# Performance work log

Hardware: AMD Instinct MI355X
Metric: run time of the kernel (lower is better)

Reference implementation:

```python
import jax, jax.numpy as jnp
import numpy as np

LN_EPS = 1e-6

def layernorm(x, w, b):
    m = jnp.mean(x, axis=-1, keepdims=True)
    v = jnp.mean((x - m) ** 2, axis=-1, keepdims=True)
    return (x - m) * jax.lax.rsqrt(v + LN_EPS) * w + b

def rotate_half(x):
    x1, x2 = jnp.split(x, 2, axis=-1)
    return jnp.concatenate([-x2, x1], axis=-1)

def headwise_lowrank(x, U, V, b):
    # x: [B,S,D], U: [H,D,r], V: [H,r,hd] -> [B,S,H*hd]
    xu = jnp.einsum('bsd,hdr->bshr', x, U)
    y = jnp.einsum('bshr,hre->bshe', xu, V)
    B, S, H, E = y.shape
    return y.reshape(B, S, H * E) + b

def setup_inputs() -> dict:
    key = jax.random.key(0)
    B, S, D, H, HD = 4, 2048, 768, 12, 64
    RA, RF, DFF = 32, 512, 3072
    ks = jax.random.split(key, 20)
    s = 0.02
    inp = {
        'x': jax.random.normal(ks[0], (B, S, D), jnp.float32),
        'attn_norm_w': jnp.ones((D,), jnp.float32),
        'attn_norm_b': jnp.zeros((D,), jnp.float32),
        'Uq': jax.random.normal(ks[1], (H, D, RA), jnp.float32) * s,
        'Vq': jax.random.normal(ks[2], (H, RA, HD), jnp.float32),
        'bq': jax.random.normal(ks[3], (D,), jnp.float32) * s,
        'Uk': jax.random.normal(ks[4], (H, D, RA), jnp.float32) * s,
        'Vk': jax.random.normal(ks[5], (H, RA, HD), jnp.float32),
        'bk': jax.random.normal(ks[6], (D,), jnp.float32) * s,
        'Uv': jax.random.normal(ks[7], (H, D, RA), jnp.float32) * s,
        'Vv': jax.random.normal(ks[8], (H, RA, HD), jnp.float32),
        'bv': jax.random.normal(ks[9], (D,), jnp.float32) * s,
        'Wo_w': jax.random.normal(ks[10], (D, D), jnp.float32) * s,
        'Wo_b': jax.random.normal(ks[11], (D,), jnp.float32) * s,
        'mlp_norm_w': jnp.ones((D,), jnp.float32),
        'mlp_norm_b': jnp.zeros((D,), jnp.float32),
        'Ui': jax.random.normal(ks[12], (D, RF), jnp.float32) * s,
        'Vi': jax.random.normal(ks[13], (RF, 2 * DFF), jnp.float32),
        'bi': jax.random.normal(ks[14], (2 * DFF,), jnp.float32) * s,
        'Uo': jax.random.normal(ks[15], (DFF, RF), jnp.float32) * s,
        'Vo': jax.random.normal(ks[16], (RF, D), jnp.float32),
        'bo': jax.random.normal(ks[17], (D,), jnp.float32) * s,
    }
    # real RoPE tables [S, HD]
    inv_freq = 1.0 / (10000.0 ** (np.arange(0, HD, 2, dtype=np.float32) / HD))
    t = np.arange(S, dtype=np.float32)
    freqs = np.outer(t, inv_freq)  # [S, HD/2]
    emb = np.concatenate([freqs, freqs], axis=-1)
    inp['cos'] = jnp.asarray(np.cos(emb))
    inp['sin'] = jnp.asarray(np.sin(emb))
    return inp

def reference(x, attn_norm_w, attn_norm_b, Uq, Vq, bq, Uk, Vk, bk, Uv, Vv, bv,
              cos, sin, Wo_w, Wo_b, mlp_norm_w, mlp_norm_b, Ui, Vi, bi, Uo, Vo, bo):
    B, S, D = x.shape
    H, HD = Vq.shape[0], Vq.shape[2]
    # --- attention sub-block (pre-norm) ---
    h = layernorm(x, attn_norm_w, attn_norm_b)
    q = headwise_lowrank(h, Uq, Vq, bq).reshape(B, S, H, HD).transpose(0, 2, 1, 3)
    k = headwise_lowrank(h, Uk, Vk, bk).reshape(B, S, H, HD).transpose(0, 2, 1, 3)
    v = headwise_lowrank(h, Uv, Vv, bv).reshape(B, S, H, HD).transpose(0, 2, 1, 3)
    c = cos[None, None]  # [1,1,S,HD]
    s_ = sin[None, None]
    q = q * c + rotate_half(q) * s_
    k = k * c + rotate_half(k) * s_
    scale = 1.0 / jnp.sqrt(jnp.asarray(HD, q.dtype))
    scores = jnp.einsum('bhqd,bhkd->bhqk', q, k) * scale
    attn = jax.nn.softmax(scores, axis=-1)
    o = jnp.einsum('bhqk,bhkd->bhqd', attn, v)
    o = o.transpose(0, 2, 1, 3).reshape(B, S, D)
    x1 = x + o @ Wo_w.T + Wo_b
    # --- FFN sub-block (pre-norm, low-rank GEGLU) ---
    h2 = layernorm(x1, mlp_norm_w, mlp_norm_b)
    u = (h2 @ Ui) @ Vi + bi  # [B,S,2*dff]
    g1, g2 = jnp.split(u, 2, axis=-1)
    g = jax.nn.gelu(g1, approximate=True) * g2
    y = (g @ Uo) @ Vo + bo
    return x1 + y
```

## Files before the change

kernel.cpp:

```cpp
#include <hip/hip_runtime.h>
#include <hip/hip_bf16.h>
#include <math.h>

#define NTOK 8192
#define SEQ  2048
#define DM   768
#define NH   12
#define HD2  64
#define RA   32
#define NG   3072

typedef __attribute__((ext_vector_type(8))) short bf16x8;
typedef __attribute__((ext_vector_type(4))) float f32x4;

__device__ __forceinline__ float b2f(unsigned short u) {
    union { unsigned int i; float f; } v; v.i = ((unsigned int)u) << 16; return v.f;
}
__device__ __forceinline__ unsigned short f2b_rne(float f) {
    union { float f; unsigned int i; } v; v.f = f;
    unsigned int b = v.i + 0x7FFFu + ((v.i >> 16) & 1u);
    return (unsigned short)(b >> 16);
}
__device__ __forceinline__ float wval(const void* p, size_t i, int bf) {
    return bf ? b2f(((const unsigned short*)p)[i]) : ((const float*)p)[i];
}
__device__ __forceinline__ unsigned int cvt_pk_bf16(float a, float b) {
    unsigned int r;
    asm("v_cvt_pk_bf16_f32 %0, %1, %2" : "=v"(r) : "v"(a), "v"(b));
    return r;
}

__global__ void detect_kernel(const unsigned int* __restrict__ w1, int* __restrict__ flag) {
    *flag = (w1[0] == 0x3F800000u) ? 0 : 1;
}

__global__ __launch_bounds__(256) void conv_f32_kernel(const void* __restrict__ src,
        float* __restrict__ dst, int n, const int* __restrict__ flag) {
    int i = blockIdx.x * 256 + threadIdx.x;
    if (i < n)
        dst[i] = (*flag) ? b2f(((const unsigned short*)src)[i]) : ((const float*)src)[i];
}

__global__ __launch_bounds__(256) void conv_b16_kernel(const void* __restrict__ src,
        unsigned short* __restrict__ dst, int n, const int* __restrict__ flag) {
    int i = blockIdx.x * 256 + threadIdx.x;
    if (i < n)
        dst[i] = (*flag) ? ((const unsigned short*)src)[i] : f2b_rne(((const float*)src)[i]);
}

__global__ __launch_bounds__(256) void conv_split_kernel(const void* __restrict__ src,
        unsigned short* __restrict__ hi, unsigned short* __restrict__ lo,
        int n, const int* __restrict__ flag) {
    int i = blockIdx.x * 256 + threadIdx.x;
    if (i < n) {
        float v = (*flag) ? b2f(((const unsigned short*)src)[i]) : ((const float*)src)[i];
        unsigned short h = f2b_rne(v);
        hi[i] = h;
        lo[i] = f2b_rne(v - b2f(h));
    }
}

__global__ __launch_bounds__(256) void ln_kernel(const float* __restrict__ x,
        const void* __restrict__ w, const void* __restrict__ b,
        void* __restrict__ out, void* __restrict__ out2,
        const int* __restrict__ flag, int mode) {
    int bf = *flag;
    int row = blockIdx.x, tid = threadIdx.x;
    const float* xr = x + (size_t)row * DM;
    float v0 = xr[tid];
    float v1 = xr[tid + 256];
    float v2 = xr[tid + 512];
    float s = v0 + v1 + v2;
    float ss = v0 * v0 + v1 * v1 + v2 * v2;
    #pragma unroll
    for (int off = 32; off >= 1; off >>= 1) {
        s  += __shfl_xor(s, off);
        ss += __shfl_xor(ss, off);
    }
    __shared__ float rs[4], rq[4];
    int wid = tid >> 6;
    if ((tid & 63) == 0) { rs[wid] = s; rq[wid] = ss; }
    __syncthreads();
    s  = rs[0] + rs[1] + rs[2] + rs[3];
    ss = rq[0] + rq[1] + rq[2] + rq[3];
    float mean = s * (1.0f / DM);
    float var  = ss * (1.0f / DM) - mean * mean;
    float inv  = rsqrtf(var + 1e-6f);
    float o0 = (v0 - mean) * inv * wval(w, tid, bf)       + wval(b, tid, bf);
    float o1 = (v1 - mean) * inv * wval(w, tid + 256, bf) + wval(b, tid + 256, bf);
    float o2 = (v2 - mean) * inv * wval(w, tid + 512, bf) + wval(b, tid + 512, bf);
    if (mode == 2) {
        unsigned short* oh = (unsigned short*)out  + (size_t)row * DM;
        unsigned short* ol = (unsigned short*)out2 + (size_t)row * DM;
        unsigned short h0 = f2b_rne(o0), h1 = f2b_rne(o1), h2 = f2b_rne(o2);
        oh[tid] = h0; oh[tid + 256] = h1; oh[tid + 512] = h2;
        ol[tid]       = f2b_rne(o0 - b2f(h0));
        ol[tid + 256] = f2b_rne(o1 - b2f(h1));
        ol[tid + 512] = f2b_rne(o2 - b2f(h2));
    } else if (mode == 1) {
        unsigned short* orow = (unsigned short*)out + (size_t)row * DM;
        orow[tid] = f2b_rne(o0); orow[tid + 256] = f2b_rne(o1); orow[tid + 512] = f2b_rne(o2);
    } else {
        float* orow = (float*)out + (size_t)row * DM;
        orow[tid] = o0; orow[tid + 256] = o1; orow[tid + 512] = o2;
    }
}

__global__ __launch_bounds__(256) void xu_mfma(
        const unsigned short* __restrict__ Ah, const unsigned short* __restrict__ Al,
        const unsigned short* __restrict__ Uh0, const unsigned short* __restrict__ Ul0,
        const unsigned short* __restrict__ Uh1, const unsigned short* __restrict__ Ul1,
        const unsigned short* __restrict__ Uh2, const unsigned short* __restrict__ Ul2,
        float* __restrict__ XU) {
    __shared__ unsigned short Ash[128][40], Asl[128][40];
    __shared__ unsigned short Bsh[128][40], Bsl[128][40];
    int tid = threadIdx.x;
    int w = tid >> 6, lane = tid & 63;
    int n16 = lane & 15, quad = lane >> 4;
    int m0 = blockIdx.x * 128, n0 = blockIdx.y * 128;
    int which = n0 / 384;
    const unsigned short* Uh = (which == 0) ? Uh0 : (which == 1) ? Uh1 : Uh2;
    const unsigned short* Ul = (which == 0) ? Ul0 : (which == 1) ? Ul1 : Ul2;
    int nh0 = n0 - which * 384;
    int mh = (w & 1) * 64, nh = (w >> 1) * 64;
    f32x4 acc[4][4] = {};

    int am = tid >> 1, akb = (tid & 1) * 16;
    const unsigned short* ahp = Ah + (size_t)(m0 + am) * DM + akb;
    const unsigned short* alp = Al + (size_t)(m0 + am) * DM + akb;
    int kp = (tid & 15) * 2, nb = (tid >> 4) * 8;
    int hc = nh0 + nb;
    int head = hc >> 5, rr = hc & 31;
    size_t bbase = (size_t)head * (DM * RA) + (size_t)kp * RA + rr;

    uint4 rah0 = *(const uint4*)ahp,       rah1 = *(const uint4*)(ahp + 8);
    uint4 ral0 = *(const uint4*)alp,       ral1 = *(const uint4*)(alp + 8);
    uint4 rbh0 = *(const uint4*)(Uh + bbase);
    uint4 rbh1 = *(const uint4*)(Uh + bbase + RA);
    uint4 rbl0 = *(const uint4*)(Ul + bbase);
    uint4 rbl1 = *(const uint4*)(Ul + bbase + RA);

    for (int k0 = 0; k0 < DM; k0 += 32) {
        __builtin_amdgcn_s_barrier();
        *(uint4*)&Ash[am][akb]     = rah0;
        *(uint4*)&Ash[am][akb + 8] = rah1;
        *(uint4*)&Asl[am][akb]     = ral0;
        *(uint4*)&Asl[am][akb + 8] = ral1;
        {
            const unsigned int* a = (const unsigned int*)&rbh0;
            const unsigned int* b = (const unsigned int*)&rbh1;
            #pragma unroll
            for (int d = 0; d < 4; d++) {
                *(unsigned int*)&Bsh[nb + 2 * d][kp]     = (a[d] & 0xFFFFu) | (b[d] << 16);
                *(unsigned int*)&Bsh[nb + 2 * d + 1][kp] = (a[d] >> 16) | (b[d] & 0xFFFF0000u);
            }
            const unsigned int* c = (const unsigned int*)&rbl0;
            const unsigned int* e = (const unsigned int*)&rbl1;
            #pragma unroll
            for (int d = 0; d < 4; d++) {
                *(unsigned int*)&Bsl[nb + 2 * d][kp]     = (c[d] & 0xFFFFu) | (e[d] << 16);
                *(unsigned int*)&Bsl[nb + 2 * d + 1][kp] = (c[d] >> 16) | (e[d] & 0xFFFF0000u);
            }
        }
        if (k0 + 32 < DM) {
            rah0 = *(const uint4*)(ahp + k0 + 32); rah1 = *(const uint4*)(ahp + k0 + 40);
            ral0 = *(const uint4*)(alp + k0 + 32); ral1 = *(const uint4*)(alp + k0 + 40);
            size_t nbb = bbase + (size_t)(k0 + 32) * RA;
            rbh0 = *(const uint4*)(Uh + nbb); rbh1 = *(const uint4*)(Uh + nbb + RA);
            rbl0 = *(const uint4*)(Ul + nbb); rbl1 = *(const uint4*)(Ul + nbb + RA);
        }
        asm volatile("s_waitcnt lgkmcnt(0)" ::: "memory");
        __builtin_amdgcn_s_barrier();
        bf16x8 ah[4], al[4], bh[4], bl[4];
        #pragma unroll
        for (int i = 0; i < 4; i++) {
            ah[i] = *(const bf16x8*)&Ash[mh + i * 16 + n16][quad * 8];
            al[i] = *(const bf16x8*)&Asl[mh + i * 16 + n16][quad * 8];
            bh[i] = *(const bf16x8*)&Bsh[nh + i * 16 + n16][quad * 8];
            bl[i] = *(const bf16x8*)&Bsl[nh + i * 16 + n16][quad * 8];
        }
        #pragma unroll
        for (int mi = 0; mi < 4; mi++)
            #pragma unroll
            for (int ni = 0; ni < 4; ni++) {
                acc[mi][ni] = __builtin_amdgcn_mfma_f32_16x16x32_bf16(ah[mi], bh[ni], acc[mi][ni], 0, 0, 0);
                acc[mi][ni] = __builtin_amdgcn_mfma_f32_16x16x32_bf16(ah[mi], bl[ni], acc[mi][ni], 0, 0, 0);
                acc[mi][ni] = __builtin_amdgcn_mfma_f32_16x16x32_bf16(al[mi], bh[ni], acc[mi][ni], 0, 0, 0);
            }
    }
    #pragma unroll
    for (int mi = 0; mi < 4; mi++)
        #pragma unroll
        for (int ni = 0; ni < 4; ni++) {
            int col = n0 + nh + ni * 16 + n16;
            #pragma unroll
            for (int r = 0; r < 4; r++) {
                int row = m0 + mh + mi * 16 + quad * 4 + r;
                XU[(size_t)row * 1152 + col] = acc[mi][ni][r];
            }
        }
}

__global__ __launch_bounds__(256) void qkv2_kernel(
        const float* __restrict__ XU,
        const void* __restrict__ Vq, const void* __restrict__ bq,
        const void* __restrict__ Vk, const void* __restrict__ bk,
        const void* __restrict__ Vv, const void* __restrict__ bv,
        const void* __restrict__ cosT, const void* __restrict__ sinT,
        unsigned short* __restrict__ qhg, unsigned short* __restrict__ qlg,
        unsigned short* __restrict__ khg, unsigned short* __restrict__ klg,
        unsigned short* __restrict__ vtg, const int* __restrict__ flag) {
    int bf = *flag;
    int tok0 = blockIdx.x * 64;
    int head = blockIdx.y;
    int tid = threadIdx.x;
    int row = tid >> 2;
    int e0  = (tid & 3) * 16;
    int tok = tok0 + row;
    int bb = tok >> 11, ssp = tok & (SEQ - 1);
    int ssp0 = tok0 & (SEQ - 1);
    int bh = bb * NH + head;
    __shared__ float XUs[64][33];
    __shared__ float Vws[32][65];
    __shared__ float obs[64][65];
    const void* Vp[3] = {Vq, Vk, Vv};
    const void* bp[3] = {bq, bk, bv};
    for (int which = 0; which < 3; which++) {
        __syncthreads();
        for (int i = tid; i < 2048; i += 256) {
            int rr = i >> 5, r = i & 31;
            XUs[rr][r] = XU[(size_t)(tok0 + rr) * 1152 + which * 384 + head * 32 + r];
        }
        for (int i = tid; i < 2048; i += 256) {
            int r = i >> 6, e = i & 63;
            Vws[r][e] = wval(Vp[which], (size_t)head * RA * HD2 + (size_t)r * 64 + e, bf);
        }
        __syncthreads();
        float acc[16];
        #pragma unroll
        for (int j = 0; j < 16; j++) acc[j] = wval(bp[which], head * 64 + e0 + j, bf);
        #pragma unroll 8
        for (int r = 0; r < 32; r++) {
            float xv = XUs[row][r];
            #pragma unroll
            for (int j = 0; j < 16; j++) acc[j] += xv * Vws[r][e0 + j];
        }
        #pragma unroll
        for (int j = 0; j < 16; j++) obs[row][e0 + j] = acc[j];
        __syncthreads();
        if (which == 2) {
            int e = tid >> 2, seg = (tid & 3) * 16;
            unsigned short buf[16];
            #pragma unroll
            for (int i = 0; i < 16; i++) buf[i] = f2b_rne(obs[seg + i][e]);
            unsigned short* dp = vtg + ((size_t)bh * 64 + e) * SEQ + ssp0 + seg;
            *(uint4*)dp = ((const uint4*)buf)[0];
            *(uint4*)(dp + 8) = ((const uint4*)buf)[1];
        } else {
            float scale = (which == 0) ? 0.18033688011112042f : 1.0f;
            unsigned short hbuf[16], lbuf[16];
            #pragma unroll
            for (int j = 0; j < 16; j++) {
                int e = e0 + j;
                float c  = wval(cosT, (size_t)ssp * 64 + e, bf);
                float sn = wval(sinT, (size_t)ssp * 64 + e, bf);
                float other = (e < 32) ? -obs[row][e + 32] : obs[row][e - 32];
                float val = (acc[j] * c + other * sn) * scale;
                unsigned short h = f2b_rne(val);
                hbuf[j] = h;
                lbuf[j] = f2b_rne(val - b2f(h));
            }
            unsigned short* hp = ((which == 0) ? qhg : khg) + ((size_t)bh * SEQ + ssp) * 64 + e0;
            unsigned short* lp = ((which == 0) ? qlg : klg) + ((size_t)bh * SEQ + ssp) * 64 + e0;
            *(uint4*)hp = ((const uint4*)hbuf)[0];
            *(uint4*)(hp + 8) = ((const uint4*)hbuf)[1];
            *(uint4*)lp = ((const uint4*)lbuf)[0];
            *(uint4*)(lp + 8) = ((const uint4*)lbuf)[1];
        }
    }
}

__global__ __launch_bounds__(256) void attn_mfma(
        const unsigned short* __restrict__ qh, const unsigned short* __restrict__ ql,
        const unsigned short* __restrict__ kh, const unsigned short* __restrict__ kl,
        const unsigned short* __restrict__ vt, unsigned short* __restrict__ og) {
    int qt = blockIdx.x, bh = blockIdx.y;
    int bb = bh / NH, hh = bh - bb * NH;
    int tid = threadIdx.x;
    int w = tid >> 6, lane = tid & 63;
    int n16 = lane & 15, quad = lane >> 4;

    __shared__ __align__(16) unsigned short Khs[64][64];
    __shared__ __align__(16) unsigned short Kls[64][64];
    __shared__ __align__(16) unsigned short VTs[64][64];
    __shared__ __align__(16) unsigned short Pbs[4][16][64];

    size_t qoff = ((size_t)bh * SEQ + qt * 64 + w * 16 + n16) * 64 + quad * 8;
    bf16x8 aqh0 = *(const bf16x8*)(qh + qoff);
    bf16x8 aqh1 = *(const bf16x8*)(qh + qoff + 32);
    bf16x8 aql0 = *(const bf16x8*)(ql + qoff);
    bf16x8 aql1 = *(const bf16x8*)(ql + qoff + 32);

    bf16x8 vones;
    #pragma unroll
    for (int i = 0; i < 8; i++) vones[i] = (short)0x3F80;

    float m[4] = {-1e30f, -1e30f, -1e30f, -1e30f};
    float l[4] = {0.f, 0.f, 0.f, 0.f};
    f32x4 O[4] = {};
    const unsigned short* kh_p = kh + (size_t)bh * SEQ * 64;
    const unsigned short* kl_p = kl + (size_t)bh * SEQ * 64;
    const unsigned short* vt_p = vt + (size_t)bh * 64 * SEQ;

    int row0 = tid >> 3, ch = tid & 7;
    int row1 = row0 + 32;
    int sw0 = (ch ^ (row0 & 7)) * 8;
    int sw1 = (ch ^ (row1 & 7)) * 8;
    size_t ko0 = (size_t)row0 * 64 + ch * 8;
    size_t ko1 = (size_t)row1 * 64 + ch * 8;
    size_t vo0 = (size_t)row0 * SEQ + ch * 8;
    size_t vo1 = (size_t)row1 * SEQ + ch * 8;

    uint4 rkh0 = *(const uint4*)(kh_p + ko0);
    uint4 rkh1 = *(const uint4*)(kh_p + ko1);
    uint4 rkl0 = *(const uint4*)(kl_p + ko0);
    uint4 rkl1 = *(const uint4*)(kl_p + ko1);
    uint4 rv0  = *(const uint4*)(vt_p + vo0);
    uint4 rv1  = *(const uint4*)(vt_p + vo1);

    int px = n16 & 7;
    int c0 = (quad ^ px) * 8;
    int c1 = ((quad + 4) ^ px) * 8;

    for (int t0 = 0; t0 < SEQ; t0 += 64) {
        __builtin_amdgcn_s_barrier();
        *(uint4*)&Khs[row0][sw0] = rkh0;
        *(uint4*)&Khs[row1][sw1] = rkh1;
        *(uint4*)&Kls[row0][sw0] = rkl0;
        *(uint4*)&Kls[row1][sw1] = rkl1;
        *(uint4*)&VTs[row0][sw0] = rv0;
        *(uint4*)&VTs[row1][sw1] = rv1;
        if (t0 + 64 < SEQ) {
            size_t kt = (size_t)(t0 + 64) * 64;
            rkh0 = *(const uint4*)(kh_p + kt + ko0);
            rkh1 = *(const uint4*)(kh_p + kt + ko1);
            rkl0 = *(const uint4*)(kl_p + kt + ko0);
            rkl1 = *(const uint4*)(kl_p + kt + ko1);
            rv0  = *(const uint4*)(vt_p + (t0 + 64) + vo0);
            rv1  = *(const uint4*)(vt_p + (t0 + 64) + vo1);
        }
        asm volatile("s_waitcnt lgkmcnt(0)" ::: "memory");
        __builtin_amdgcn_s_barrier();

        f32x4 s[4];
        #pragma unroll
        for (int t = 0; t < 4; t++) {
            int rr = 16 * t + n16;
            bf16x8 bkh0 = *(const bf16x8*)&Khs[rr][c0];
            bf16x8 bkh1 = *(const bf16x8*)&Khs[rr][c1];
            bf16x8 bkl0 = *(const bf16x8*)&Kls[rr][c0];
            bf16x8 bkl1 = *(const bf16x8*)&Kls[rr][c1];
            f32x4 a = {};
            a = __builtin_amdgcn_mfma_f32_16x16x32_bf16(aqh0, bkh0, a, 0, 0, 0);
            a = __builtin_amdgcn_mfma_f32_16x16x32_bf16(aqh1, bkh1, a, 0, 0, 0);
            a = __builtin_amdgcn_mfma_f32_16x16x32_bf16(aqh0, bkl0, a, 0, 0, 0);
            a = __builtin_amdgcn_mfma_f32_16x16x32_bf16(aqh1, bkl1, a, 0, 0, 0);
            a = __builtin_amdgcn_mfma_f32_16x16x32_bf16(aql0, bkh0, a, 0, 0, 0);
            a = __builtin_amdgcn_mfma_f32_16x16x32_bf16(aql1, bkh1, a, 0, 0, 0);
            s[t] = a;
        }
        float mt[4];
        #pragma unroll
        for (int r = 0; r < 4; r++) {
            float v = fmaxf(fmaxf(s[0][r], s[1][r]), fmaxf(s[2][r], s[3][r]));
            v = fmaxf(v, __shfl_xor(v, 1));
            v = fmaxf(v, __shfl_xor(v, 2));
            v = fmaxf(v, __shfl_xor(v, 4));
            v = fmaxf(v, __shfl_xor(v, 8));
            mt[r] = v;
        }
        float need = fmaxf(fmaxf(mt[0] - m[0], mt[1] - m[1]),
                           fmaxf(mt[2] - m[2], mt[3] - m[3]));
        if (__any(need > 8.0f)) {
            #pragma unroll
            for (int r = 0; r < 4; r++) {
                float mn = fmaxf(m[r], mt[r]);
                float al = exp2f(m[r] - mn);
                m[r] = mn;
                l[r] *= al;
                #pragma unroll
                for (int t2 = 0; t2 < 4; t2++) O[t2][r] *= al;
            }
        }
        int qr = quad * 4;
        #pragma unroll
        for (int t = 0; t < 4; t++) {
            float p0 = exp2f(s[t][0] - m[0]);
            float p1 = exp2f(s[t][1] - m[1]);
            float p2 = exp2f(s[t][2] - m[2]);
            float p3 = exp2f(s[t][3] - m[3]);
            unsigned int pk01 = cvt_pk_bf16(p0, p1);
            unsigned int pk23 = cvt_pk_bf16(p2, p3);
            int cb = 2 * t + (n16 >> 3);
            Pbs[w][qr + 0][((cb ^ ((qr + 0) & 7)) << 3) | px] = (unsigned short)pk01;
            Pbs[w][qr + 1][((cb ^ ((qr + 1) & 7)) << 3) | px] = (unsigned short)(pk01 >> 16);
            Pbs[w][qr + 2][((cb ^ ((qr + 2) & 7)) << 3) | px] = (unsigned short)pk23;
            Pbs[w][qr + 3][((cb ^ ((qr + 3) & 7)) << 3) | px] = (unsigned short)(pk23 >> 16);
        }
        bf16x8 ap0 = *(const bf16x8*)&Pbs[w][n16][c0];
        bf16x8 ap1 = *(const bf16x8*)&Pbs[w][n16][c1];
        f32x4 ls = {};
        ls = __builtin_amdgcn_mfma_f32_16x16x32_bf16(ap0, vones, ls, 0, 0, 0);
        ls = __builtin_amdgcn_mfma_f32_16x16x32_bf16(ap1, vones, ls, 0, 0, 0);
        #pragma unroll
        for (int r = 0; r < 4; r++) l[r] += ls[r];
        #pragma unroll
        for (int t2 = 0; t2 < 4; t2++) {
            bf16x8 bv0 = *(const bf16x8*)&VTs[16 * t2 + n16][c0];
            bf16x8 bv1 = *(const bf16x8*)&VTs[16 * t2 + n16][c1];
            O[t2] = __builtin_amdgcn_mfma_f32_16x16x32_bf16(ap0, bv0, O[t2], 0, 0, 0);
            O[t2] = __builtin_amdgcn_mfma_f32_16x16x32_bf16(ap1, bv1, O[t2], 0, 0, 0);
        }
    }
    int srow = qt * 64 + w * 16 + quad * 4;
    #pragma unroll
    for (int r = 0; r < 4; r++) {
        float inv = 1.0f / l[r];
        unsigned short* op = og + ((size_t)bb * SEQ + srow + r) * DM + hh * HD2 + n16;
        #pragma unroll
        for (int t2 = 0; t2 < 4; t2++)
            op[16 * t2] = f2b_rne(O[t2][r] * inv);
    }
}

template <int MODE, bool TB>
__global__ __launch_bounds__(512) void gemm_bf16(
        const unsigned short* __restrict__ A, const unsigned short* __restrict__ Bw,
        const void* __restrict__ bias, const float* __restrict__ resid,
        void* __restrict__ Cout, int Nn, int K, const int* __restrict__ flag) {
    __shared__ unsigned short As[128][40];
    __shared__ unsigned short Bs[128][40];
    int tid = threadIdx.x;
    int w = tid >> 6, lane = tid & 63;
    int n16 = lane & 15, quad = lane >> 4;
    int m0 = blockIdx.x * 128, n0 = blockIdx.y * 128;
    int mh = (w & 3) * 32, nh = (w >> 2) * 64;
    f32x4 acc[2][4] = {};

    int st = tid & 255;
    bool isA = tid < 256;
    int am = st >> 1, akb = (st & 1) * 16;
    int bkp = (st & 15) * 2, bnb = (st >> 4) * 8;
    int bn = st >> 1, bkb = (st & 1) * 16;
    const unsigned short* gp0;
    const unsigned short* gp1;
    if (isA) {
        gp0 = A + (size_t)(m0 + am) * K + akb;
        gp1 = gp0 + 8;
    } else if (!TB) {
        gp0 = Bw + (size_t)bkp * Nn + n0 + bnb;
        gp1 = gp0 + Nn;
    } else {
        gp0 = Bw + (size_t)(n0 + bn) * K + bkb;
        gp1 = gp0 + 8;
    }
    uint4 r0 = *(const uint4*)gp0;
    uint4 r1 = *(const uint4*)gp1;

    for (int k0 = 0; k0 < K; k0 += 32) {
        __builtin_amdgcn_s_barrier();
        if (isA) {
            *(uint4*)&As[am][akb]     = r0;
            *(uint4*)&As[am][akb + 8] = r1;
        } else if (!TB) {
            const unsigned int* a = (const unsigned int*)&r0;
            const unsigned int* b = (const unsigned int*)&r1;
            #pragma unroll
            for (int d = 0; d < 4; d++) {
                *(unsigned int*)&Bs[bnb + 2 * d][bkp]     = (a[d] & 0xFFFFu) | (b[d] << 16);
                *(unsigned int*)&Bs[bnb + 2 * d + 1][bkp] = (a[d] >> 16) | (b[d] & 0xFFFF0000u);
            }
        } else {
            *(uint4*)&Bs[bn][bkb]     = r0;
            *(uint4*)&Bs[bn][bkb + 8] = r1;
        }
        if (k0 + 32 < K) {
            size_t adv = (isA || TB) ? (size_t)(k0 + 32) : (size_t)(k0 + 32) * Nn;
            r0 = *(const uint4*)(gp0 + adv);
            r1 = *(const uint4*)(gp1 + adv);
        }
        asm volatile("s_waitcnt lgkmcnt(0)" ::: "memory");
        __builtin_amdgcn_s_barrier();
        bf16x8 af[2], bfr[4];
        #pragma unroll
        for (int i = 0; i < 2; i++)
            af[i] = *(const bf16x8*)&As[mh + i * 16 + n16][quad * 8];
        #pragma unroll
        for (int i = 0; i < 4; i++)
            bfr[i] = *(const bf16x8*)&Bs[nh + i * 16 + n16][quad * 8];
        #pragma unroll
        for (int mi = 0; mi < 2; mi++)
            #pragma unroll
            for (int ni = 0; ni < 4; ni++)
                acc[mi][ni] = __builtin_amdgcn_mfma_f32_16x16x32_bf16(af[mi], bfr[ni], acc[mi][ni], 0, 0, 0);
    }
    int bf = (MODE == 0) ? 0 : *flag;
    #pragma unroll
    for (int ni = 0; ni < 4; ni++) {
        int col = n0 + nh + ni * 16 + n16;
        float bv = (MODE == 0) ? 0.f : wval(bias, col, bf);
        #pragma unroll
        for (int mi = 0; mi < 2; mi++) {
            #pragma unroll
            for (int r = 0; r < 4; r++) {
                int row = m0 + mh + mi * 16 + quad * 4 + r;
                float val = acc[mi][ni][r];
                if constexpr (MODE == 0) {
                    ((unsigned short*)Cout)[(size_t)row * Nn + col] = f2b_rne(val);
                } else if constexpr (MODE == 1) {
                    ((float*)Cout)[(size_t)row * Nn + col] =
                        val + bv + resid[(size_t)row * Nn + col];
                } else {
                    float o = val + bv + resid[(size_t)row * Nn + col];
                    if (bf)
                        ((unsigned short*)Cout)[(size_t)row * Nn + col] = f2b_rne(o);
                    else
                        ((float*)Cout)[(size_t)row * Nn + col] = o;
                }
            }
        }
    }
}

__global__ __launch_bounds__(256) void geglu_bf16(
        const unsigned short* __restrict__ A, const unsigned short* __restrict__ Bw,
        const void* __restrict__ bias, unsigned short* __restrict__ G,
        const int* __restrict__ flag) {
    int bf = *flag;
    const int K = 512, Nn = 2 * NG;
    __shared__ unsigned short As[128][40];
    __shared__ unsigned short B1s[64][40];
    __shared__ unsigned short B2s[64][40];
    int tid = threadIdx.x;
    int w = tid >> 6, lane = tid & 63;
    int n16 = lane & 15, quad = lane >> 4;
    int m0 = blockIdx.x * 128, n0 = blockIdx.y * 64;
    int mh = (w & 1) * 64;
    int nq = (w >> 1) * 32;
    f32x4 acc1[4][2] = {}, acc2[4][2] = {};

    int am = tid >> 1, akb = (tid & 1) * 16;
    const unsigned short* aptr = A + (size_t)(m0 + am) * K + akb;
    uint4 ra0 = *(const uint4*)aptr;
    uint4 ra1 = *(const uint4*)(aptr + 8);
    int t_ = tid & 127, hsel = tid >> 7;
    int bkp = (t_ & 15) * 2, bnb = (t_ >> 4) * 8;
    const unsigned short* bptr = Bw + (size_t)bkp * Nn + n0 + (size_t)hsel * NG + bnb;
    uint4 rb0 = *(const uint4*)bptr;
    uint4 rb1 = *(const uint4*)(bptr + Nn);

    for (int k0 = 0; k0 < K; k0 += 32) {
        __builtin_amdgcn_s_barrier();
        *(uint4*)&As[am][akb]     = ra0;
        *(uint4*)&As[am][akb + 8] = ra1;
        {
            const unsigned int* a = (const unsigned int*)&rb0;
            const unsigned int* b = (const unsigned int*)&rb1;
            unsigned short (*Bst)[40] = hsel ? B2s : B1s;
            #pragma unroll
            for (int d = 0; d < 4; d++) {
                *(unsigned int*)&Bst[bnb + 2 * d][bkp]     = (a[d] & 0xFFFFu) | (b[d] << 16);
                *(unsigned int*)&Bst[bnb + 2 * d + 1][bkp] = (a[d] >> 16) | (b[d] & 0xFFFF0000u);
            }
        }
        if (k0 + 32 < K) {
            ra0 = *(const uint4*)(aptr + k0 + 32);
            ra1 = *(const uint4*)(aptr + k0 + 40);
            const unsigned short* nbp = bptr + (size_t)(k0 + 32) * Nn;
            rb0 = *(const uint4*)nbp;
            rb1 = *(const uint4*)(nbp + Nn);
        }
        asm volatile("s_waitcnt lgkmcnt(0)" ::: "memory");
        __builtin_amdgcn_s_barrier();
        bf16x8 af[4], b1f[2], b2f_[2];
        #pragma unroll
        for (int i = 0; i < 4; i++)
            af[i] = *(const bf16x8*)&As[mh + i * 16 + n16][quad * 8];
        #pragma unroll
        for (int i = 0; i < 2; i++) {
            b1f[i]  = *(const bf16x8*)&B1s[nq + i * 16 + n16][quad * 8];
            b2f_[i] = *(const bf16x8*)&B2s[nq + i * 16 + n16][quad * 8];
        }
        #pragma unroll
        for (int mi = 0; mi < 4; mi++)
            #pragma unroll
            for (int ni = 0; ni < 2; ni++) {
                acc1[mi][ni] = __builtin_amdgcn_mfma_f32_16x16x32_bf16(af[mi], b1f[ni], acc1[mi][ni], 0, 0, 0);
                acc2[mi][ni] = __builtin_amdgcn_mfma_f32_16x16x32_bf16(af[mi], b2f_[ni], acc2[mi][ni], 0, 0, 0);
            }
    }
    #pragma unroll
    for (int ni = 0; ni < 2; ni++) {
        int ccol = nq + ni * 16 + n16;
        float b1 = wval(bias, n0 + ccol, bf);
        float b2 = wval(bias, NG + n0 + ccol, bf);
        #pragma unroll
        for (int mi = 0; mi < 4; mi++) {
            #pragma unroll
            for (int r = 0; r < 4; r++) {
                int rrow = mh + mi * 16 + quad * 4 + r;
                float u1 = acc1[mi][ni][r] + b1;
                float u2 = acc2[mi][ni][r] + b2;
                float nz = fminf(-2.3022083f * (u1 + 0.044715f * u1 * u1 * u1), 126.f);
                float gl = u1 * __builtin_amdgcn_rcpf(1.0f + exp2f(nz));
                G[(size_t)(m0 + rrow) * NG + n0 + ccol] = f2b_rne(gl * u2);
            }
        }
    }
}

extern "C" void kernel_launch(void* const* d_in, const int* in_sizes, int n_in,
                              void* d_out, int out_size, void* d_ws, size_t ws_size,
                              hipStream_t stream) {
    (void)in_sizes; (void)n_in; (void)out_size; (void)ws_size;
    const size_t ND = (size_t)NTOK * DM;
    const int USZ = NH * DM * RA;

    float* ws = (float*)d_ws;
    int*   flag = (int*)d_ws;
    float* xf = ws + 256;
    float* P0 = xf + ND;
    float* P1 = P0 + ND;
    float* P2 = P1 + ND;
    float* P3 = P2 + ND;
    float* P4 = P3 + ND;
    float* P5 = P4 + ND;
    float* XU = P4;

    unsigned short* hH = (unsigned short*)P0;
    unsigned short* hL = hH + ND;
    unsigned short* qhb = (unsigned short*)P1;
    unsigned short* qlb = qhb + ND;
    unsigned short* khb = qhb + 2 * ND;
    unsigned short* klb = qhb + 3 * ND;
    unsigned short* vtb = qhb + 4 * ND;
    unsigned short* ob  = (unsigned short*)P0;
    unsigned short* h2b = (unsigned short*)P1;
    unsigned short* tb  = (unsigned short*)P2;
    unsigned short* gb  = (unsigned short*)P3;
    unsigned short* t2b = (unsigned short*)P0;
    unsigned short* wb  = (unsigned short*)(P5 + ND);
    unsigned short* WoB = wb;
    unsigned short* UiB = WoB + 589824;
    unsigned short* ViB = UiB + 393216;
    unsigned short* UoB = ViB + 3145728;
    unsigned short* VoB = UoB + 1572864;
    unsigned short* UqH = VoB + 393216;
    unsigned short* UqL = UqH + USZ;
    unsigned short* UkH = UqL + USZ;
    unsigned short* UkL = UkH + USZ;
    unsigned short* UvH = UkL + USZ;
    unsigned short* UvL = UvH + USZ;

    detect_kernel<<<1, 1, 0, stream>>>((const unsigned int*)d_in[1], flag);
    conv_f32_kernel<<<(int)((ND + 255) / 256), 256, 0, stream>>>(d_in[0], xf, (int)ND, flag);
    conv_b16_kernel<<<(589824 + 255) / 256, 256, 0, stream>>>(d_in[12], WoB, 589824, flag);
    conv_b16_kernel<<<(393216 + 255) / 256, 256, 0, stream>>>(d_in[16], UiB, 393216, flag);
    conv_b16_kernel<<<(3145728 + 255) / 256, 256, 0, stream>>>(d_in[17], ViB, 3145728, flag);
    conv_b16_kernel<<<(1572864 + 255) / 256, 256, 0, stream>>>(d_in[19], UoB, 1572864, flag);
    conv_b16_kernel<<<(393216 + 255) / 256, 256, 0, stream>>>(d_in[20], VoB, 393216, flag);
    conv_split_kernel<<<(USZ + 255) / 256, 256, 0, stream>>>(d_in[3], UqH, UqL, USZ, flag);
    conv_split_kernel<<<(USZ + 255) / 256, 256, 0, stream>>>(d_in[6], UkH, UkL, USZ, flag);
    conv_split_kernel<<<(USZ + 255) / 256, 256, 0, stream>>>(d_in[9], UvH, UvL, USZ, flag);

    ln_kernel<<<NTOK, 256, 0, stream>>>(xf, d_in[1], d_in[2], hH, hL, flag, 2);
    xu_mfma<<<dim3(64, 9), 256, 0, stream>>>(hH, hL, UqH, UqL, UkH, UkL, UvH, UvL, XU);
    qkv2_kernel<<<dim3(NTOK / 64, NH), 256, 0, stream>>>(XU,
                                         d_in[4], d_in[5], d_in[7], d_in[8],
                                         d_in[10], d_in[11], d_in[22], d_in[23],
                                         qhb, qlb, khb, klb, vtb, flag);
    attn_mfma<<<dim3(SEQ / 64, 4 * NH), 256, 0, stream>>>(qhb, qlb, khb, klb, vtb, ob);
    gemm_bf16<1, true><<<dim3(64, 6), 512, 0, stream>>>(ob, WoB, d_in[13], xf,
                                                        (void*)P5, DM, DM, flag);
    ln_kernel<<<NTOK, 256, 0, stream>>>(P5, d_in[14], d_in[15], (void*)h2b, nullptr, flag, 1);
    gemm_bf16<0, false><<<dim3(64, 4), 512, 0, stream>>>(h2b, UiB, nullptr, nullptr,
                                                         (void*)tb, 512, DM, flag);
    geglu_bf16<<<dim3(64, 48), 256, 0, stream>>>(tb, ViB, d_in[18], gb, flag);
    gemm_bf16<0, false><<<dim3(64, 4), 512, 0, stream>>>(gb, UoB, nullptr, nullptr,
                                                         (void*)t2b, 512, NG, flag);
    gemm_bf16<3, false><<<dim3(64, 6), 512, 0, stream>>>(t2b, VoB, d_in[21], P5,
                                                         d_out, DM, 512, flag);
}
```

Baseline: 740.2 us.

## Drop split-bf16 Q/K in attention and widen GEGLU tiles to 128x128

Q and K are now stored as a single bf16 value instead of a hi/lo bf16 pair, so the attention score loop issues 2 MFMAs per tile instead of 6, with half the K shared-memory staging and global traffic. Separately, the GEGLU GEMM uses 512-thread blocks with 128-wide N tiles and dedicated loader threads for A and B, halving the grid. The precision reduction in QK^T may raise numerical error in the attention scores against the fp32 reference.

```diff
diff --git a/kernel.cpp b/kernel.cpp
--- a/kernel.cpp
+++ b/kernel.cpp
@@ -207,8 +207,7 @@
         const void* __restrict__ Vk, const void* __restrict__ bk,
         const void* __restrict__ Vv, const void* __restrict__ bv,
         const void* __restrict__ cosT, const void* __restrict__ sinT,
-        unsigned short* __restrict__ qhg, unsigned short* __restrict__ qlg,
-        unsigned short* __restrict__ khg, unsigned short* __restrict__ klg,
+        unsigned short* __restrict__ qg, unsigned short* __restrict__ kg,
         unsigned short* __restrict__ vtg, const int* __restrict__ flag) {
     int bf = *flag;
     int tok0 = blockIdx.x * 64;
@@ -258,7 +257,7 @@
             *(uint4*)(dp + 8) = ((const uint4*)buf)[1];
         } else {
             float scale = (which == 0) ? 0.18033688011112042f : 1.0f;
-            unsigned short hbuf[16], lbuf[16];
+            unsigned short hbuf[16];
             #pragma unroll
             for (int j = 0; j < 16; j++) {
                 int e = e0 + j;
@@ -266,23 +265,17 @@
                 float sn = wval(sinT, (size_t)ssp * 64 + e, bf);
                 float other = (e < 32) ? -obs[row][e + 32] : obs[row][e - 32];
                 float val = (acc[j] * c + other * sn) * scale;
-                unsigned short h = f2b_rne(val);
-                hbuf[j] = h;
-                lbuf[j] = f2b_rne(val - b2f(h));
-            }
-            unsigned short* hp = ((which == 0) ? qhg : khg) + ((size_t)bh * SEQ + ssp) * 64 + e0;
-            unsigned short* lp = ((which == 0) ? qlg : klg) + ((size_t)bh * SEQ + ssp) * 64 + e0;
+                hbuf[j] = f2b_rne(val);
+            }
+            unsigned short* hp = ((which == 0) ? qg : kg) + ((size_t)bh * SEQ + ssp) * 64 + e0;
             *(uint4*)hp = ((const uint4*)hbuf)[0];
             *(uint4*)(hp + 8) = ((const uint4*)hbuf)[1];
-            *(uint4*)lp = ((const uint4*)lbuf)[0];
-            *(uint4*)(lp + 8) = ((const uint4*)lbuf)[1];
         }
     }
 }
 
 __global__ __launch_bounds__(256) void attn_mfma(
-        const unsigned short* __restrict__ qh, const unsigned short* __restrict__ ql,
-        const unsigned short* __restrict__ kh, const unsigned short* __restrict__ kl,
+        const unsigned short* __restrict__ qg, const unsigned short* __restrict__ kg,
         const unsigned short* __restrict__ vt, unsigned short* __restrict__ og) {
     int qt = blockIdx.x, bh = blockIdx.y;
     int bb = bh / NH, hh = bh - bb * NH;
@@ -291,15 +284,12 @@
     int n16 = lane & 15, quad = lane >> 4;
 
     __shared__ __align__(16) unsigned short Khs[64][64];
-    __shared__ __align__(16) unsigned short Kls[64][64];
     __shared__ __align__(16) unsigned short VTs[64][64];
     __shared__ __align__(16) unsigned short Pbs[4][16][64];
 
     size_t qoff = ((size_t)bh * SEQ + qt * 64 + w * 16 + n16) * 64 + quad * 8;
-    bf16x8 aqh0 = *(const bf16x8*)(qh + qoff);
-    bf16x8 aqh1 = *(const bf16x8*)(qh + qoff + 32);
-    bf16x8 aql0 = *(const bf16x8*)(ql + qoff);
-    bf16x8 aql1 = *(const bf16x8*)(ql + qoff + 32);
+    bf16x8 aq0 = *(const bf16x8*)(qg + qoff);
+    bf16x8 aq1 = *(const bf16x8*)(qg + qoff + 32);
 
     bf16x8 vones;
     #pragma unroll
@@ -308,8 +298,7 @@
     float m[4] = {-1e30f, -1e30f, -1e30f, -1e30f};
     float l[4] = {0.f, 0.f, 0.f, 0.f};
     f32x4 O[4] = {};
-    const unsigned short* kh_p = kh + (size_t)bh * SEQ * 64;
-    const unsigned short* kl_p = kl + (size_t)bh * SEQ * 64;
+    const unsigned short* k_p  = kg + (size_t)bh * SEQ * 64;
     const unsigned short* vt_p = vt + (size_t)bh * 64 * SEQ;
 
     int row0 = tid >> 3, ch = tid & 7;
@@ -321,12 +310,10 @@
     size_t vo0 = (size_t)row0 * SEQ + ch * 8;
     size_t vo1 = (size_t)row1 * SEQ + ch * 8;
 
-    uint4 rkh0 = *(const uint4*)(kh_p + ko0);
-    uint4 rkh1 = *(const uint4*)(kh_p + ko1);
-    uint4 rkl0 = *(const uint4*)(kl_p + ko0);
-    uint4 rkl1 = *(const uint4*)(kl_p + ko1);
-    uint4 rv0  = *(const uint4*)(vt_p + vo0);
-    uint4 rv1  = *(const uint4*)(vt_p + vo1);
+    uint4 rk0 = *(const uint4*)(k_p + ko0);
+    uint4 rk1 = *(const uint4*)(k_p + ko1);
+    uint4 rv0 = *(const uint4*)(vt_p + vo0);
+    uint4 rv1 = *(const uint4*)(vt_p + vo1);
 
     int px = n16 & 7;
     int c0 = (quad ^ px) * 8;
@@ -334,20 +321,16 @@
 
     for (int t0 = 0; t0 < SEQ; t0 += 64) {
         __builtin_amdgcn_s_barrier();
-        *(uint4*)&Khs[row0][sw0] = rkh0;
-        *(uint4*)&Khs[row1][sw1] = rkh1;
-        *(uint4*)&Kls[row0][sw0] = rkl0;
-        *(uint4*)&Kls[row1][sw1] = rkl1;
+        *(uint4*)&Khs[row0][sw0] = rk0;
+        *(uint4*)&Khs[row1][sw1] = rk1;
         *(uint4*)&VTs[row0][sw0] = rv0;
         *(uint4*)&VTs[row1][sw1] = rv1;
         if (t0 + 64 < SEQ) {
             size_t kt = (size_t)(t0 + 64) * 64;
-            rkh0 = *(const uint4*)(kh_p + kt + ko0);
-            rkh1 = *(const uint4*)(kh_p + kt + ko1);
-            rkl0 = *(const uint4*)(kl_p + kt + ko0);
-            rkl1 = *(const uint4*)(kl_p + kt + ko1);
-            rv0  = *(const uint4*)(vt_p + (t0 + 64) + vo0);
-            rv1  = *(const uint4*)(vt_p + (t0 + 64) + vo1);
+            rk0 = *(const uint4*)(k_p + kt + ko0);
+            rk1 = *(const uint4*)(k_p + kt + ko1);
+            rv0 = *(const uint4*)(vt_p + (t0 + 64) + vo0);
+            rv1 = *(const uint4*)(vt_p + (t0 + 64) + vo1);
         }
         asm volatile("s_waitcnt lgkmcnt(0)" ::: "memory");
         __builtin_amdgcn_s_barrier();
@@ -356,17 +339,11 @@
         #pragma unroll
         for (int t = 0; t < 4; t++) {
             int rr = 16 * t + n16;
-            bf16x8 bkh0 = *(const bf16x8*)&Khs[rr][c0];
-            bf16x8 bkh1 = *(const bf16x8*)&Khs[rr][c1];
-            bf16x8 bkl0 = *(const bf16x8*)&Kls[rr][c0];
-            bf16x8 bkl1 = *(const bf16x8*)&Kls[rr][c1];
+            bf16x8 bk0 = *(const bf16x8*)&Khs[rr][c0];
+            bf16x8 bk1 = *(const bf16x8*)&Khs[rr][c1];
             f32x4 a = {};
-            a = __builtin_amdgcn_mfma_f32_16x16x32_bf16(aqh0, bkh0, a, 0, 0, 0);
-            a = __builtin_amdgcn_mfma_f32_16x16x32_bf16(aqh1, bkh1, a, 0, 0, 0);
-            a = __builtin_amdgcn_mfma_f32_16x16x32_bf16(aqh0, bkl0, a, 0, 0, 0);
-            a = __builtin_amdgcn_mfma_f32_16x16x32_bf16(aqh1, bkl1, a, 0, 0, 0);
-            a = __builtin_amdgcn_mfma_f32_16x16x32_bf16(aql0, bkh0, a, 0, 0, 0);
-            a = __builtin_amdgcn_mfma_f32_16x16x32_bf16(aql1, bkh1, a, 0, 0, 0);
+            a = __builtin_amdgcn_mfma_f32_16x16x32_bf16(aq0, bk0, a, 0, 0, 0);
+            a = __builtin_amdgcn_mfma_f32_16x16x32_bf16(aq1, bk1, a, 0, 0, 0);
             s[t] = a;
         }
         float mt[4];
@@ -532,88 +509,110 @@
     }
 }
 
-__global__ __launch_bounds__(256) void geglu_bf16(
+__global__ __launch_bounds__(512) void geglu_bf16(
         const unsigned short* __restrict__ A, const unsigned short* __restrict__ Bw,
         const void* __restrict__ bias, unsigned short* __restrict__ G,
         const int* __restrict__ flag) {
     int bf = *flag;
     const int K = 512, Nn = 2 * NG;
     __shared__ unsigned short As[128][40];
-    __shared__ unsigned short B1s[64][40];
-    __shared__ unsigned short B2s[64][40];
+    __shared__ unsigned short B1s[128][40];
+    __shared__ unsigned short B2s[128][40];
     int tid = threadIdx.x;
     int w = tid >> 6, lane = tid & 63;
     int n16 = lane & 15, quad = lane >> 4;
-    int m0 = blockIdx.x * 128, n0 = blockIdx.y * 64;
-    int mh = (w & 1) * 64;
-    int nq = (w >> 1) * 32;
-    f32x4 acc1[4][2] = {}, acc2[4][2] = {};
-
-    int am = tid >> 1, akb = (tid & 1) * 16;
-    const unsigned short* aptr = A + (size_t)(m0 + am) * K + akb;
-    uint4 ra0 = *(const uint4*)aptr;
-    uint4 ra1 = *(const uint4*)(aptr + 8);
-    int t_ = tid & 127, hsel = tid >> 7;
+    int m0 = blockIdx.x * 128, n0 = blockIdx.y * 128;
+    int mh = (w & 3) * 32, nh = (w >> 2) * 64;
+    f32x4 acc1[2][4] = {}, acc2[2][4] = {};
+
+    bool isA = tid < 256;
+    int st = tid & 255;
+    int am = st >> 1, akb = (st & 1) * 16;
+    int t_ = tid & 127, hsel = (tid & 255) >> 7;
     int bkp = (t_ & 15) * 2, bnb = (t_ >> 4) * 8;
-    const unsigned short* bptr = Bw + (size_t)bkp * Nn + n0 + (size_t)hsel * NG + bnb;
-    uint4 rb0 = *(const uint4*)bptr;
-    uint4 rb1 = *(const uint4*)(bptr + Nn);
+    const unsigned short* gpa;
+    const unsigned short* gpb;
+    uint4 r0, r1, r2, r3;
+    if (isA) {
+        gpa = A + (size_t)(m0 + am) * K + akb;
+        r0 = *(const uint4*)gpa;
+        r1 = *(const uint4*)(gpa + 8);
+    } else {
+        gpb = Bw + (size_t)bkp * Nn + n0 + (size_t)hsel * NG + bnb;
+        r0 = *(const uint4*)gpb;
+        r1 = *(const uint4*)(gpb + Nn);
+        r2 = *(const uint4*)(gpb + 64);
+        r3 = *(const uint4*)(gpb + Nn + 64);
+    }
 
     for (int k0 = 0; k0 < K; k0 += 32) {
         __builtin_amdgcn_s_barrier();
-        *(uint4*)&As[am][akb]     = ra0;
-        *(uint4*)&As[am][akb + 8] = ra1;
-        {
-            const unsigned int* a = (const unsigned int*)&rb0;
-            const unsigned int* b = (const unsigned int*)&rb1;
+        if (isA) {
+            *(uint4*)&As[am][akb]     = r0;
+            *(uint4*)&As[am][akb + 8] = r1;
+        } else {
             unsigned short (*Bst)[40] = hsel ? B2s : B1s;
+            const unsigned int* a = (const unsigned int*)&r0;
+            const unsigned int* b = (const unsigned int*)&r1;
             #pragma unroll
             for (int d = 0; d < 4; d++) {
                 *(unsigned int*)&Bst[bnb + 2 * d][bkp]     = (a[d] & 0xFFFFu) | (b[d] << 16);
                 *(unsigned int*)&Bst[bnb + 2 * d + 1][bkp] = (a[d] >> 16) | (b[d] & 0xFFFF0000u);
             }
+            const unsigned int* c = (const unsigned int*)&r2;
+            const unsigned int* e = (const unsigned int*)&r3;
+            #pragma unroll
+            for (int d = 0; d < 4; d++) {
+                *(unsigned int*)&Bst[bnb + 64 + 2 * d][bkp]     = (c[d] & 0xFFFFu) | (e[d] << 16);
+                *(unsigned int*)&Bst[bnb + 64 + 2 * d + 1][bkp] = (c[d] >> 16) | (e[d] & 0xFFFF0000u);
+            }
         }
         if (k0 + 32 < K) {
-            ra0 = *(const uint4*)(aptr + k0 + 32);
-            ra1 = *(const uint4*)(aptr + k0 + 40);
-            const unsigned short* nbp = bptr + (size_t)(k0 + 32) * Nn;
-            rb0 = *(const uint4*)nbp;
-            rb1 = *(const uint4*)(nbp + Nn);
+            if (isA) {
+                r0 = *(const uint4*)(gpa + k0 + 32);
+                r1 = *(const uint4*)(gpa + k0 + 40);
+            } else {
+                const unsigned short* nbp = gpb + (size_t)(k0 + 32) * Nn;
+                r0 = *(const uint4*)nbp;
+                r1 = *(const uint4*)(nbp + Nn);
+                r2 = *(const uint4*)(nbp + 64);
+                r3 = *(const uint4*)(nbp + Nn + 64);
+            }
         }
         asm volatile("s_waitcnt lgkmcnt(0)" ::: "memory");
         __builtin_amdgcn_s_barrier();
-        bf16x8 af[4], b1f[2], b2f_[2];
-        #pragma unroll
-        for (int i = 0; i < 4; i++)
+        bf16x8 af[2], b1f[4], b2f_[4];
+        #pragma unroll
+        for (int i = 0; i < 2; i++)
             af[i] = *(const bf16x8*)&As[mh + i * 16 + n16][quad * 8];
         #pragma unroll
-        for (int i = 0; i < 2; i++) {
-            b1f[i]  = *(const bf16x8*)&B1s[nq + i * 16 + n16][quad * 8];
-            b2f_[i] = *(const bf16x8*)&B2s[nq + i * 16 + n16][quad * 8];
-        }
-        #pragma unroll
-        for (int mi = 0; mi < 4; mi++)
-            #pragma unroll
-            for (int ni = 0; ni < 2; ni++) {
+        for (int i = 0; i < 4; i++) {
+            b1f[i]  = *(const bf16x8*)&B1s[nh + i * 16 + n16][quad * 8];
+            b2f_[i] = *(const bf16x8*)&B2s[nh + i * 16 + n16][quad * 8];
+        }
+        #pragma unroll
+        for (int mi = 0; mi < 2; mi++)
+            #pragma unroll
+            for (int ni = 0; ni < 4; ni++) {
                 acc1[mi][ni] = __builtin_amdgcn_mfma_f32_16x16x32_bf16(af[mi], b1f[ni], acc1[mi][ni], 0, 0, 0);
                 acc2[mi][ni] = __builtin_amdgcn_mfma_f32_16x16x32_bf16(af[mi], b2f_[ni], acc2[mi][ni], 0, 0, 0);
             }
     }
     #pragma unroll
-    for (int ni = 0; ni < 2; ni++) {
-        int ccol = nq + ni * 16 + n16;
-        float b1 = wval(bias, n0 + ccol, bf);
-        float b2 = wval(bias, NG + n0 + ccol, bf);
-        #pragma unroll
-        for (int mi = 0; mi < 4; mi++) {
+    for (int ni = 0; ni < 4; ni++) {
+        int col = n0 + nh + ni * 16 + n16;
+        float b1 = wval(bias, col, bf);
+        float b2 = wval(bias, NG + col, bf);
+        #pragma unroll
+        for (int mi = 0; mi < 2; mi++) {
             #pragma unroll
             for (int r = 0; r < 4; r++) {
-                int rrow = mh + mi * 16 + quad * 4 + r;
+                int row = mh + mi * 16 + quad * 4 + r;
                 float u1 = acc1[mi][ni][r] + b1;
                 float u2 = acc2[mi][ni][r] + b2;
                 float nz = fminf(-2.3022083f * (u1 + 0.044715f * u1 * u1 * u1), 126.f);
                 float gl = u1 * __builtin_amdgcn_rcpf(1.0f + exp2f(nz));
-                G[(size_t)(m0 + rrow) * NG + n0 + ccol] = f2b_rne(gl * u2);
+                G[(size_t)(m0 + row) * NG + col] = f2b_rne(gl * u2);
             }
         }
     }
@@ -639,11 +638,9 @@
 
     unsigned short* hH = (unsigned short*)P0;
     unsigned short* hL = hH + ND;
-    unsigned short* qhb = (unsigned short*)P1;
-    unsigned short* qlb = qhb + ND;
-    unsigned short* khb = qhb + 2 * ND;
-    unsigned short* klb = qhb + 3 * ND;
-    unsigned short* vtb = qhb + 4 * ND;
+    unsigned short* qb  = (unsigned short*)P1;
+    unsigned short* kb  = qb + ND;
+    unsigned short* vtb = qb + 2 * ND;
     unsigned short* ob  = (unsigned short*)P0;
     unsigned short* h2b = (unsigned short*)P1;
     unsigned short* tb  = (unsigned short*)P2;
@@ -678,14 +675,14 @@
     qkv2_kernel<<<dim3(NTOK / 64, NH), 256, 0, stream>>>(XU,
                                          d_in[4], d_in[5], d_in[7], d_in[8],
                                          d_in[10], d_in[11], d_in[22], d_in[23],
-                                         qhb, qlb, khb, klb, vtb, flag);
-    attn_mfma<<<dim3(SEQ / 64, 4 * NH), 256, 0, stream>>>(qhb, qlb, khb, klb, vtb, ob);
+                                         qb, kb, vtb, flag);
+    attn_mfma<<<dim3(SEQ / 64, 4 * NH), 256, 0, stream>>>(qb, kb, vtb, ob);
     gemm_bf16<1, true><<<dim3(64, 6), 512, 0, stream>>>(ob, WoB, d_in[13], xf,
                                                         (void*)P5, DM, DM, flag);
     ln_kernel<<<NTOK, 256, 0, stream>>>(P5, d_in[14], d_in[15], (void*)h2b, nullptr, flag, 1);
     gemm_bf16<0, false><<<dim3(64, 4), 512, 0, stream>>>(h2b, UiB, nullptr, nullptr,
                                                          (void*)tb, 512, DM, flag);
-    geglu_bf16<<<dim3(64, 48), 256, 0, stream>>>(tb, ViB, d_in[18], gb, flag);
+    geglu_bf16<<<dim3(64, 24), 512, 0, stream>>>(tb, ViB, d_in[18], gb, flag);
     gemm_bf16<0, false><<<dim3(64, 4), 512, 0, stream>>>(gb, UoB, nullptr, nullptr,
                                                          (void*)t2b, 512, NG, flag);
     gemm_bf16<3, false><<<dim3(64, 6), 512, 0, stream>>>(t2b, VoB, d_in[21], P5,
```

New measurement: 743.6 us. Within noise of the previous version (+0.5%).
